# Kernel optimization log

Measured on AMD Instinct MI355X. Metric: run time of the kernel, lower is better.

## Reference

```python
import jax, jax.numpy as jnp
import numpy as np

N_NODES = 50000
N_EDGES = 800000
N_GRAPHS = 512
IN_DIM, HID, OUT_DIM = 128, 96, 10
N_CONV = 4


def setup_inputs() -> dict:
    key = jax.random.key(0)
    ks = jax.random.split(key, 16)
    s = 0.05
    inp = {
        "x": jax.random.normal(ks[0], (N_NODES, IN_DIM), dtype=jnp.float32),
        "edge_index": jax.random.randint(ks[1], (2, N_EDGES), 0, N_NODES, dtype=jnp.int64),
        "batch": jnp.sort(jax.random.randint(ks[2], (N_NODES,), 0, N_GRAPHS, dtype=jnp.int64)),
        # encoder MLP (2 layers: in->hid, hid->hid)
        "enc_W0": jax.random.normal(ks[3], (IN_DIM, HID), dtype=jnp.float32) * s,
        "enc_b0": jnp.zeros((HID,), dtype=jnp.float32),
        "enc_W1": jax.random.normal(ks[4], (HID, HID), dtype=jnp.float32) * s,
        "enc_b1": jnp.zeros((HID,), dtype=jnp.float32),
        # stacked GCNConv weights
        "conv_W": jax.random.normal(ks[5], (N_CONV, HID, HID), dtype=jnp.float32) * s,
        "conv_b": jnp.zeros((N_CONV, HID), dtype=jnp.float32),
        # decoder MLP (2 layers: hid->hid, hid->out)
        "dec_W0": jax.random.normal(ks[6], (HID, HID), dtype=jnp.float32) * s,
        "dec_b0": jnp.zeros((HID,), dtype=jnp.float32),
        "dec_W1": jax.random.normal(ks[7], (HID, OUT_DIM), dtype=jnp.float32) * s,
        "dec_b1": jnp.zeros((OUT_DIM,), dtype=jnp.float32),
    }
    return inp


def reference(x, edge_index, batch, enc_W0, enc_b0, enc_W1, enc_b1,
              conv_W, conv_b, dec_W0, dec_b0, dec_W1, dec_b1):
    n = x.shape[0]
    src, dst = edge_index[0], edge_index[1]  # source_to_target flow

    # encoder MLP (dropout is identity in eval mode)
    h = jax.nn.relu(x @ enc_W0 + enc_b0)
    h = h @ enc_W1 + enc_b1

    # GCN symmetric normalization with self-loops: deg[i] = in_degree + 1
    deg = jax.ops.segment_sum(jnp.ones_like(dst, dtype=h.dtype), dst, num_segments=n) + 1.0
    dinv = jax.lax.rsqrt(deg)                    # [N]
    edge_norm = (dinv[src] * dinv[dst])[:, None]  # [E,1]
    self_norm = (dinv * dinv)[:, None]            # [N,1] self-loop coefficient

    for l in range(conv_W.shape[0]):
        hw = h @ conv_W[l]                              # linear transform [N,HID]
        msg = hw[src] * edge_norm                       # gather + scale [E,HID]
        h = (jax.ops.segment_sum(msg, dst, num_segments=n)
             + hw * self_norm + conv_b[l])              # scatter-add + self-loop + bias
        h = jax.nn.relu(h)

    # global add pool over graphs in the batch
    g = jax.ops.segment_sum(h, batch, num_segments=N_GRAPHS)  # [G,HID]

    # decoder MLP
    g = jax.nn.relu(g @ dec_W0 + dec_b0)
    return g @ dec_W1 + dec_b1
```

## Files before the change

kernel.cpp:

```cpp
#include <hip/hip_runtime.h>

#define HID 96
#define INDIM 128
#define OUTDIM 10

typedef __attribute__((ext_vector_type(8))) short bf16x8;
typedef __attribute__((ext_vector_type(4))) float f32x4;

__device__ __forceinline__ unsigned short f2bf(float f) {
  unsigned int u = __float_as_uint(f);
  unsigned int r = (u + 0x7FFFu + ((u >> 16) & 1u)) >> 16;
  return (unsigned short)r;
}
__device__ __forceinline__ bf16x8 as_bf16x8(uint4 u) {
  union { uint4 a; bf16x8 b; } c; c.a = u; return c.b;
}
__device__ __forceinline__ float bflo(unsigned int u) { return __uint_as_float(u << 16); }
__device__ __forceinline__ float bfhi(unsigned int u) { return __uint_as_float(u & 0xFFFF0000u); }

__global__ __launch_bounds__(256) void k_prep(const float* __restrict__ x,
                                              unsigned int* __restrict__ xb, long long xu,
                                              int* __restrict__ cnt, int n, int XB,
                                              const float* __restrict__ encW0,
                                              const float* __restrict__ encW1,
                                              const float* __restrict__ convW,
                                              uint4* __restrict__ wp) {
  int b = blockIdx.x;
  if (b < XB) {
    long long i = (long long)b * 256 + threadIdx.x;
    if (i < xu) {
      float2 v = ((const float2*)x)[i];
      xb[i] = (unsigned int)f2bf(v.x) | ((unsigned int)f2bf(v.y) << 16);
    }
    if (i < n) cnt[i] = 0;
    return;
  }
  int bid = b - XB;
  int lane = threadIdx.x;
  if (lane >= 64) return;
  const float* Wsrc;
  int frag;
  if (bid < 24) { Wsrc = encW0; frag = bid; }
  else if (bid < 42) { Wsrc = encW1; frag = bid - 24; }
  else { int c = bid - 42; Wsrc = convW + (size_t)(c / 18) * HID * HID; frag = c % 18; }
  int ks = frag / 6, cf = frag % 6;
  int col = cf * 16 + (lane & 15);
  int k0 = ks * 32 + (lane >> 4) * 8;
  unsigned int u[4];
#pragma unroll
  for (int p = 0; p < 4; ++p) {
    float lo = Wsrc[(size_t)(k0 + 2 * p) * 96 + col];
    float hi = Wsrc[(size_t)(k0 + 2 * p + 1) * 96 + col];
    u[p] = (unsigned int)f2bf(lo) | ((unsigned int)f2bf(hi) << 16);
  }
  uint4 r; r.x = u[0]; r.y = u[1]; r.z = u[2]; r.w = u[3];
  wp[(size_t)bid * 64 + lane] = r;
}

__global__ void k_count(const int4* __restrict__ dst4, int E4, int* __restrict__ cnt,
                        int* __restrict__ rank) {
  int i = blockIdx.x * 256 + threadIdx.x;
  if (i >= E4) return;
  int4 d = dst4[i];
  int r0 = atomicAdd(&cnt[d.x], 1);
  int r1 = atomicAdd(&cnt[d.y], 1);
  int r2 = atomicAdd(&cnt[d.z], 1);
  int r3 = atomicAdd(&cnt[d.w], 1);
  ((int4*)rank)[i] = make_int4(r0, r1, r2, r3);
}

__global__ __launch_bounds__(256) void k_scanA(const int* __restrict__ cnt, int n,
                                               int* __restrict__ bsum,
                                               float* __restrict__ dinv) {
  __shared__ int red[256];
  int b = blockIdx.x, t = threadIdx.x;
  int base = b * 512;
  int v = 0;
  int i0 = base + t, i1 = base + 256 + t;
  if (i0 < n) { int c = cnt[i0]; v += c; dinv[i0] = rsqrtf((float)c + 1.0f); }
  if (i1 < n) { int c = cnt[i1]; v += c; dinv[i1] = rsqrtf((float)c + 1.0f); }
  red[t] = v;
  __syncthreads();
  for (int off = 128; off > 0; off >>= 1) {
    if (t < off) red[t] += red[t + off];
    __syncthreads();
  }
  if (t == 0) bsum[b] = red[0];
}

__global__ __launch_bounds__(256) void k_scanB(const int* __restrict__ bsum, int nb,
                                               int* __restrict__ boff,
                                               int* __restrict__ rowp, int n) {
  __shared__ int s[256];
  int t = threadIdx.x;
  int v = (t < nb) ? bsum[t] : 0;
  s[t] = v;
  __syncthreads();
  for (int off = 1; off < 256; off <<= 1) {
    int u = (t >= off) ? s[t - off] : 0;
    __syncthreads();
    s[t] += u;
    __syncthreads();
  }
  if (t < nb) boff[t] = s[t] - v;
  if (t == 255) rowp[n] = s[255];
}

__global__ __launch_bounds__(256) void k_scanC(const int* __restrict__ cnt, int n,
                                               const int* __restrict__ boff,
                                               int* __restrict__ rowp) {
  __shared__ int s[256];
  int b = blockIdx.x, t = threadIdx.x;
  int base = b * 512;
  int i0 = base + 2 * t, i1 = i0 + 1;
  int c0 = (i0 < n) ? cnt[i0] : 0;
  int c1 = (i1 < n) ? cnt[i1] : 0;
  int pair = c0 + c1;
  s[t] = pair;
  __syncthreads();
  for (int off = 1; off < 256; off <<= 1) {
    int u = (t >= off) ? s[t - off] : 0;
    __syncthreads();
    s[t] += u;
    __syncthreads();
  }
  int excl = s[t] - pair + boff[b];
  if (i0 < n) rowp[i0] = excl;
  if (i1 < n) rowp[i1] = excl + c0;
}

__global__ void k_fill(const int4* __restrict__ src4, const int4* __restrict__ dst4,
                       const int4* __restrict__ rank4, int E4,
                       const int* __restrict__ rowp, int* __restrict__ csr) {
  int i = blockIdx.x * 256 + threadIdx.x;
  if (i >= E4) return;
  int4 s = src4[i];
  int4 d = dst4[i];
  int4 r = rank4[i];
  csr[rowp[d.x] + r.x] = s.x;
  csr[rowp[d.y] + r.y] = s.y;
  csr[rowp[d.z] + r.z] = s.z;
  csr[rowp[d.w] + r.w] = s.w;
}

template <int KS, bool RELU, bool BIAS, bool SCALE>
__global__ __launch_bounds__(256) void mfma_gemm(const uint4* __restrict__ Ab,
                                                 const uint4* __restrict__ Bp,
                                                 const float* __restrict__ bias,
                                                 const float* __restrict__ rowscale,
                                                 unsigned int* __restrict__ outB, int M) {
  int t = threadIdx.x, wid = t >> 6, lane = t & 63;
  int rowbase = blockIdx.x * 64 + wid * 16;
  int arow = rowbase + (lane & 15);
  if (arow >= M) arow = M - 1;
  constexpr int RU4 = KS * 4;

  f32x4 acc[6];
#pragma unroll
  for (int cf = 0; cf < 6; ++cf)
#pragma unroll
    for (int j = 0; j < 4; ++j) acc[cf][j] = 0.f;

#pragma unroll
  for (int ks = 0; ks < KS; ++ks) {
    uint4 a = Ab[(size_t)arow * RU4 + ks * 4 + (lane >> 4)];
    bf16x8 af = as_bf16x8(a);
#pragma unroll
    for (int cf = 0; cf < 6; ++cf) {
      uint4 b = Bp[(size_t)(ks * 6 + cf) * 64 + lane];
      acc[cf] = __builtin_amdgcn_mfma_f32_16x16x32_bf16(af, as_bf16x8(b), acc[cf], 0, 0, 0);
    }
  }

  int rows[4]; float rs[4];
#pragma unroll
  for (int i = 0; i < 4; ++i) {
    rows[i] = rowbase + (lane >> 4) * 4 + i;
    int cr = rows[i] < M ? rows[i] : M - 1;
    rs[i] = SCALE ? rowscale[cr] : 1.f;
  }
#pragma unroll
  for (int cf = 0; cf < 6; ++cf) {
    int col = cf * 16 + (lane & 15);
    float bv = BIAS ? bias[col] : 0.f;
#pragma unroll
    for (int i = 0; i < 4; ++i) {
      float v = acc[cf][i] + bv;
      if (RELU) v = fmaxf(v, 0.f);
      v *= rs[i];
      float p = __shfl_xor(v, 1);
      if (!(lane & 1) && rows[i] < M) {
        unsigned int u = (unsigned int)f2bf(v) | ((unsigned int)f2bf(p) << 16);
        outB[(size_t)rows[i] * 48 + cf * 8 + ((lane & 15) >> 1)] = u;
      }
    }
  }
}

__global__ __launch_bounds__(256) void k_agg(const unsigned int* __restrict__ hw_s,
                                             const int* __restrict__ rowp,
                                             const int* __restrict__ csr,
                                             const float* __restrict__ dinv,
                                             const float* __restrict__ bias,
                                             unsigned int* __restrict__ outB, int n) {
  int wave = threadIdx.x >> 6;
  int lane = threadIdx.x & 63;
  int node = blockIdx.x * 4 + wave;
  if (node >= n) return;
  int beg = rowp[node], end = rowp[node + 1];
  float acc0 = 0.f, acc1 = 0.f;
  bool act = lane < 48;
  int li = act ? lane : 0;
  int e = beg;
  for (; e + 8 <= end; e += 8) {
    unsigned int u0 = hw_s[(size_t)csr[e + 0] * 48 + li];
    unsigned int u1 = hw_s[(size_t)csr[e + 1] * 48 + li];
    unsigned int u2 = hw_s[(size_t)csr[e + 2] * 48 + li];
    unsigned int u3 = hw_s[(size_t)csr[e + 3] * 48 + li];
    unsigned int u4 = hw_s[(size_t)csr[e + 4] * 48 + li];
    unsigned int u5 = hw_s[(size_t)csr[e + 5] * 48 + li];
    unsigned int u6 = hw_s[(size_t)csr[e + 6] * 48 + li];
    unsigned int u7 = hw_s[(size_t)csr[e + 7] * 48 + li];
    acc0 += bflo(u0) + bflo(u1) + bflo(u2) + bflo(u3) +
            bflo(u4) + bflo(u5) + bflo(u6) + bflo(u7);
    acc1 += bfhi(u0) + bfhi(u1) + bfhi(u2) + bfhi(u3) +
            bfhi(u4) + bfhi(u5) + bfhi(u6) + bfhi(u7);
  }
  for (; e + 4 <= end; e += 4) {
    unsigned int u0 = hw_s[(size_t)csr[e + 0] * 48 + li];
    unsigned int u1 = hw_s[(size_t)csr[e + 1] * 48 + li];
    unsigned int u2 = hw_s[(size_t)csr[e + 2] * 48 + li];
    unsigned int u3 = hw_s[(size_t)csr[e + 3] * 48 + li];
    acc0 += bflo(u0) + bflo(u1) + bflo(u2) + bflo(u3);
    acc1 += bfhi(u0) + bfhi(u1) + bfhi(u2) + bfhi(u3);
  }
  for (; e < end; ++e) {
    unsigned int u = hw_s[(size_t)csr[e] * 48 + li];
    acc0 += bflo(u);
    acc1 += bfhi(u);
  }
  if (act) {
    float di = dinv[node];
    unsigned int us = hw_s[(size_t)node * 48 + li];
    float2 bv = ((const float2*)bias)[li];
    float r0 = fmaxf(di * (acc0 + bflo(us)) + bv.x, 0.f);
    float r1 = fmaxf(di * (acc1 + bfhi(us)) + bv.y, 0.f);
    outB[(size_t)node * 48 + li] = (unsigned int)f2bf(r0) | ((unsigned int)f2bf(r1) << 16);
  }
}

__global__ __launch_bounds__(256) void k_head(const unsigned int* __restrict__ hb,
                                              const int* __restrict__ batch, int n,
                                              const float* __restrict__ W0,
                                              const float* __restrict__ b0,
                                              const float* __restrict__ W1,
                                              const float* __restrict__ b1,
                                              float* __restrict__ out) {
  __shared__ float w0L[HID * HID];
  __shared__ float red[4][HID];
  __shared__ float g1L[HID];
  __shared__ float g2L[HID];
  int gr = blockIdx.x;
  int t = threadIdx.x, wv = t >> 6, lane = t & 63;

  for (int i = t; i < HID * HID / 4; i += 256) ((float4*)w0L)[i] = ((const float4*)W0)[i];

  int lo = 0, hi = n;
  while (lo < hi) { int m = (lo + hi) >> 1; if (batch[m] < gr) lo = m + 1; else hi = m; }
  int start = lo;
  hi = n;
  while (lo < hi) { int m = (lo + hi) >> 1; if (batch[m] < gr + 1) lo = m + 1; else hi = m; }
  int end = lo;

  if (lane < 48) {
    float s0 = 0.f, s1 = 0.f;
    for (int i = start + wv; i < end; i += 4) {
      unsigned int u = hb[(size_t)i * 48 + lane];
      s0 += bflo(u);
      s1 += bfhi(u);
    }
    red[wv][2 * lane] = s0;
    red[wv][2 * lane + 1] = s1;
  }
  __syncthreads();
  if (t < HID) g1L[t] = red[0][t] + red[1][t] + red[2][t] + red[3][t];
  __syncthreads();
  if (t < HID) {
    float a = b0[t];
    for (int k = 0; k < HID; ++k) a += g1L[k] * w0L[k * HID + t];
    g2L[t] = fmaxf(a, 0.f);
  }
  __syncthreads();
  if (t < OUTDIM) {
    float a = b1[t];
    for (int k = 0; k < HID; ++k) a += g2L[k] * W1[k * OUTDIM + t];
    out[(size_t)gr * OUTDIM + t] = a;
  }
}

extern "C" void kernel_launch(void* const* d_in, const int* in_sizes, int n_in,
                              void* d_out, int out_size, void* d_ws, size_t ws_size,
                              hipStream_t stream) {
  const float* x     = (const float*)d_in[0];
  const int*   ei    = (const int*)d_in[1];
  const int*   batch = (const int*)d_in[2];
  const float* encW0 = (const float*)d_in[3];
  const float* encb0 = (const float*)d_in[4];
  const float* encW1 = (const float*)d_in[5];
  const float* encb1 = (const float*)d_in[6];
  const float* convW = (const float*)d_in[7];
  const float* convb = (const float*)d_in[8];
  const float* decW0 = (const float*)d_in[9];
  const float* decb0 = (const float*)d_in[10];
  const float* decW1 = (const float*)d_in[11];
  const float* decb1 = (const float*)d_in[12];
  float* out = (float*)d_out;

  int n  = in_sizes[0] / INDIM;
  int E  = in_sizes[1] / 2;
  int G  = out_size / OUTDIM;
  int NC = in_sizes[7] / (HID * HID);

  const int* srcI = ei;
  const int* dstI = ei + E;

  char* w = (char*)d_ws;
  auto alloc = [&](size_t bytes) {
    char* p = w;
    w += (bytes + 255) & ~(size_t)255;
    return p;
  };
  unsigned int* xb  = (unsigned int*)alloc((size_t)n * (INDIM / 2) * 4);
  unsigned int* hbA = (unsigned int*)alloc((size_t)n * 48 * 4);
  unsigned int* hbB = (unsigned int*)alloc((size_t)n * 48 * 4);
  unsigned int* hwb = (unsigned int*)alloc((size_t)n * 48 * 4);
  uint4* wp   = (uint4*)alloc((size_t)(42 + NC * 18) * 64 * 16);
  int*   cnt   = (int*)alloc((size_t)n * 4);
  int*   rankb = (int*)alloc((size_t)E * 4);
  int*   rowp  = (int*)alloc((size_t)(n + 1) * 4);
  int*   csr   = (int*)alloc((size_t)E * 4);
  float* dinv  = (float*)alloc((size_t)n * 4);
  int*   bsum  = (int*)alloc(256 * 4);
  int*   boff  = (int*)alloc(256 * 4);

  long long xu = (long long)n * (INDIM / 2);
  int XB = (int)((xu + 255) / 256);
  int WB = 42 + NC * 18;
  k_prep<<<XB + WB, 256, 0, stream>>>(x, xb, xu, cnt, n, XB, encW0, encW1, convW, wp);

  int E4 = E / 4;
  int eb4 = (E4 + 255) / 256;
  int nb = (n + 511) / 512;
  k_count<<<eb4, 256, 0, stream>>>((const int4*)dstI, E4, cnt, rankb);
  k_scanA<<<nb, 256, 0, stream>>>(cnt, n, bsum, dinv);
  k_scanB<<<1, 256, 0, stream>>>(bsum, nb, boff, rowp, n);
  k_scanC<<<nb, 256, 0, stream>>>(cnt, n, boff, rowp);
  k_fill<<<eb4, 256, 0, stream>>>((const int4*)srcI, (const int4*)dstI,
                                  (const int4*)rankb, E4, rowp, csr);

  int gb = (n + 63) / 64;
  mfma_gemm<4, true, true, false><<<gb, 256, 0, stream>>>(
      (const uint4*)xb, wp, encb0, nullptr, hbA, n);
  mfma_gemm<3, false, true, false><<<gb, 256, 0, stream>>>(
      (const uint4*)hbA, wp + (size_t)24 * 64, encb1, nullptr, hbB, n);
  for (int l = 0; l < NC; ++l) {
    mfma_gemm<3, false, false, true><<<gb, 256, 0, stream>>>(
        (const uint4*)hbB, wp + (size_t)(42 + l * 18) * 64, nullptr, dinv, hwb, n);
    k_agg<<<(n + 3) / 4, 256, 0, stream>>>(hwb, rowp, csr, dinv,
                                           convb + (size_t)l * HID, hbB, n);
  }
  k_head<<<G, 256, 0, stream>>>(hbB, batch, n, decW0, decb0, decW1, decb1, out);
}
```

Baseline: 276.7 us.

## Co-schedule CSR build stages with encoder and first conv GEMMs in merged launches

Graph preprocessing kernels (count, scanA, scanC) are merged with independent dense GEMMs (encoder layers and the first conv transform) into combined grids, using block-index dispatch. This removes three launches and lets the latency-bound atomic and scan work overlap with MFMA work. The aggregation inner loop is also widened from 8 to 16 gathered neighbors per iteration for more memory-level parallelism. The cost is higher register pressure in the aggregation kernel, and mixed-role blocks sharing one launch configuration.

```diff
diff --git a/kernel.cpp b/kernel.cpp
--- a/kernel.cpp
+++ b/kernel.cpp
@@ -57,9 +57,9 @@
   wp[(size_t)bid * 64 + lane] = r;
 }
 
-__global__ void k_count(const int4* __restrict__ dst4, int E4, int* __restrict__ cnt,
-                        int* __restrict__ rank) {
-  int i = blockIdx.x * 256 + threadIdx.x;
+__device__ __forceinline__ void count_body(int blk, const int4* __restrict__ dst4, int E4,
+                                           int* __restrict__ cnt, int* __restrict__ rank) {
+  int i = blk * 256 + threadIdx.x;
   if (i >= E4) return;
   int4 d = dst4[i];
   int r0 = atomicAdd(&cnt[d.x], 1);
@@ -69,12 +69,11 @@
   ((int4*)rank)[i] = make_int4(r0, r1, r2, r3);
 }
 
-__global__ __launch_bounds__(256) void k_scanA(const int* __restrict__ cnt, int n,
-                                               int* __restrict__ bsum,
-                                               float* __restrict__ dinv) {
+__device__ __forceinline__ void scanA_body(int blk, const int* __restrict__ cnt, int n,
+                                           int* __restrict__ bsum, float* __restrict__ dinv) {
   __shared__ int red[256];
-  int b = blockIdx.x, t = threadIdx.x;
-  int base = b * 512;
+  int t = threadIdx.x;
+  int base = blk * 512;
   int v = 0;
   int i0 = base + t, i1 = base + 256 + t;
   if (i0 < n) { int c = cnt[i0]; v += c; dinv[i0] = rsqrtf((float)c + 1.0f); }
@@ -85,7 +84,121 @@
     if (t < off) red[t] += red[t + off];
     __syncthreads();
   }
-  if (t == 0) bsum[b] = red[0];
+  if (t == 0) bsum[blk] = red[0];
+}
+
+__device__ __forceinline__ void scanC_body(int blk, const int* __restrict__ cnt, int n,
+                                           const int* __restrict__ boff,
+                                           int* __restrict__ rowp) {
+  __shared__ int s[256];
+  int t = threadIdx.x;
+  int base = blk * 512;
+  int i0 = base + 2 * t, i1 = i0 + 1;
+  int c0 = (i0 < n) ? cnt[i0] : 0;
+  int c1 = (i1 < n) ? cnt[i1] : 0;
+  int pair = c0 + c1;
+  s[t] = pair;
+  __syncthreads();
+  for (int off = 1; off < 256; off <<= 1) {
+    int u = (t >= off) ? s[t - off] : 0;
+    __syncthreads();
+    s[t] += u;
+    __syncthreads();
+  }
+  int excl = s[t] - pair + boff[blk];
+  if (i0 < n) rowp[i0] = excl;
+  if (i1 < n) rowp[i1] = excl + c0;
+}
+
+template <int KS, bool RELU, bool BIAS, bool SCALE>
+__device__ __forceinline__ void gemm_body(int blk, const uint4* __restrict__ Ab,
+                                          const uint4* __restrict__ Bp,
+                                          const float* __restrict__ bias,
+                                          const float* __restrict__ rowscale,
+                                          unsigned int* __restrict__ outB, int M) {
+  int t = threadIdx.x, wid = t >> 6, lane = t & 63;
+  int rowbase = blk * 64 + wid * 16;
+  int arow = rowbase + (lane & 15);
+  if (arow >= M) arow = M - 1;
+  constexpr int RU4 = KS * 4;
+
+  f32x4 acc[6];
+#pragma unroll
+  for (int cf = 0; cf < 6; ++cf)
+#pragma unroll
+    for (int j = 0; j < 4; ++j) acc[cf][j] = 0.f;
+
+#pragma unroll
+  for (int ks = 0; ks < KS; ++ks) {
+    uint4 a = Ab[(size_t)arow * RU4 + ks * 4 + (lane >> 4)];
+    bf16x8 af = as_bf16x8(a);
+#pragma unroll
+    for (int cf = 0; cf < 6; ++cf) {
+      uint4 b = Bp[(size_t)(ks * 6 + cf) * 64 + lane];
+      acc[cf] = __builtin_amdgcn_mfma_f32_16x16x32_bf16(af, as_bf16x8(b), acc[cf], 0, 0, 0);
+    }
+  }
+
+  int rows[4]; float rs[4];
+#pragma unroll
+  for (int i = 0; i < 4; ++i) {
+    rows[i] = rowbase + (lane >> 4) * 4 + i;
+    int cr = rows[i] < M ? rows[i] : M - 1;
+    rs[i] = SCALE ? rowscale[cr] : 1.f;
+  }
+#pragma unroll
+  for (int cf = 0; cf < 6; ++cf) {
+    int col = cf * 16 + (lane & 15);
+    float bv = BIAS ? bias[col] : 0.f;
+#pragma unroll
+    for (int i = 0; i < 4; ++i) {
+      float v = acc[cf][i] + bv;
+      if (RELU) v = fmaxf(v, 0.f);
+      v *= rs[i];
+      float p = __shfl_xor(v, 1);
+      if (!(lane & 1) && rows[i] < M) {
+        unsigned int u = (unsigned int)f2bf(v) | ((unsigned int)f2bf(p) << 16);
+        outB[(size_t)rows[i] * 48 + cf * 8 + ((lane & 15) >> 1)] = u;
+      }
+    }
+  }
+}
+
+__global__ __launch_bounds__(256) void k_count_enc1(
+    const int4* __restrict__ dst4, int E4, int* __restrict__ cnt, int* __restrict__ rank,
+    int CB, const uint4* __restrict__ Ab, const uint4* __restrict__ Bp,
+    const float* __restrict__ bias, unsigned int* __restrict__ outB, int M) {
+  int b = blockIdx.x;
+  if (b < CB) count_body(b, dst4, E4, cnt, rank);
+  else gemm_body<4, true, true, false>(b - CB, Ab, Bp, bias, nullptr, outB, M);
+}
+
+__global__ __launch_bounds__(256) void k_scanA_enc2(
+    const int* __restrict__ cnt, int n, int* __restrict__ bsum, float* __restrict__ dinv,
+    int SB, const uint4* __restrict__ Ab, const uint4* __restrict__ Bp,
+    const float* __restrict__ bias, unsigned int* __restrict__ outB, int M) {
+  int b = blockIdx.x;
+  if (b < SB) scanA_body(b, cnt, n, bsum, dinv);
+  else gemm_body<3, false, true, false>(b - SB, Ab, Bp, bias, nullptr, outB, M);
+}
+
+__global__ __launch_bounds__(256) void k_scanC_conv(
+    const int* __restrict__ cnt, int n, const int* __restrict__ boff,
+    int* __restrict__ rowp, int SB, const uint4* __restrict__ Ab,
+    const uint4* __restrict__ Bp, const float* __restrict__ rowscale,
+    unsigned int* __restrict__ outB, int M) {
+  int b = blockIdx.x;
+  if (b < SB) scanC_body(b, cnt, n, boff, rowp);
+  else gemm_body<3, false, false, true>(b - SB, Ab, Bp, nullptr, rowscale, outB, M);
+}
+
+template <int KS, bool RELU, bool BIAS, bool SCALE>
+__global__ __launch_bounds__(256) void mfma_gemm(const uint4* __restrict__ Ab,
+                                                 const uint4* __restrict__ Bp,
+                                                 const float* __restrict__ bias,
+                                                 const float* __restrict__ rowscale,
+                                                 unsigned int* __restrict__ outB, int M) {
+  gemm_body<KS, RELU, BIAS, SCALE>(blockIdx.x, Ab, Bp, bias, rowscale, outB, M);
 }
 
 __global__ __launch_bounds__(256) void k_scanB(const int* __restrict__ bsum, int nb,
@@ -104,29 +217,6 @@
   }
   if (t < nb) boff[t] = s[t] - v;
   if (t == 255) rowp[n] = s[255];
-}
-
-__global__ __launch_bounds__(256) void k_scanC(const int* __restrict__ cnt, int n,
-                                               const int* __restrict__ boff,
-                                               int* __restrict__ rowp) {
-  __shared__ int s[256];
-  int b = blockIdx.x, t = threadIdx.x;
-  int base = b * 512;
-  int i0 = base + 2 * t, i1 = i0 + 1;
-  int c0 = (i0 < n) ? cnt[i0] : 0;
-  int c1 = (i1 < n) ? cnt[i1] : 0;
-  int pair = c0 + c1;
-  s[t] = pair;
-  __syncthreads();
-  for (int off = 1; off < 256; off <<= 1) {
-    int u = (t >= off) ? s[t - off] : 0;
-    __syncthreads();
-    s[t] += u;
-    __syncthreads();
-  }
-  int excl = s[t] - pair + boff[b];
-  if (i0 < n) rowp[i0] = excl;
-  if (i1 < n) rowp[i1] = excl + c0;
 }
 
 __global__ void k_fill(const int4* __restrict__ src4, const int4* __restrict__ dst4,
@@ -141,60 +231,6 @@
   csr[rowp[d.y] + r.y] = s.y;
   csr[rowp[d.z] + r.z] = s.z;
   csr[rowp[d.w] + r.w] = s.w;
-}
-
-template <int KS, bool RELU, bool BIAS, bool SCALE>
-__global__ __launch_bounds__(256) void mfma_gemm(const uint4* __restrict__ Ab,
-                                                 const uint4* __restrict__ Bp,
-                                                 const float* __restrict__ bias,
-                                                 const float* __restrict__ rowscale,
-                                                 unsigned int* __restrict__ outB, int M) {
-  int t = threadIdx.x, wid = t >> 6, lane = t & 63;
-  int rowbase = blockIdx.x * 64 + wid * 16;
-  int arow = rowbase + (lane & 15);
-  if (arow >= M) arow = M - 1;
-  constexpr int RU4 = KS * 4;
-
-  f32x4 acc[6];
-#pragma unroll
-  for (int cf = 0; cf < 6; ++cf)
-#pragma unroll
-    for (int j = 0; j < 4; ++j) acc[cf][j] = 0.f;
-
-#pragma unroll
-  for (int ks = 0; ks < KS; ++ks) {
-    uint4 a = Ab[(size_t)arow * RU4 + ks * 4 + (lane >> 4)];
-    bf16x8 af = as_bf16x8(a);
-#pragma unroll
-    for (int cf = 0; cf < 6; ++cf) {
-      uint4 b = Bp[(size_t)(ks * 6 + cf) * 64 + lane];
-      acc[cf] = __builtin_amdgcn_mfma_f32_16x16x32_bf16(af, as_bf16x8(b), acc[cf], 0, 0, 0);
-    }
-  }
-
-  int rows[4]; float rs[4];
-#pragma unroll
-  for (int i = 0; i < 4; ++i) {
-    rows[i] = rowbase + (lane >> 4) * 4 + i;
-    int cr = rows[i] < M ? rows[i] : M - 1;
-    rs[i] = SCALE ? rowscale[cr] : 1.f;
-  }
-#pragma unroll
-  for (int cf = 0; cf < 6; ++cf) {
-    int col = cf * 16 + (lane & 15);
-    float bv = BIAS ? bias[col] : 0.f;
-#pragma unroll
-    for (int i = 0; i < 4; ++i) {
-      float v = acc[cf][i] + bv;
-      if (RELU) v = fmaxf(v, 0.f);
-      v *= rs[i];
-      float p = __shfl_xor(v, 1);
-      if (!(lane & 1) && rows[i] < M) {
-        unsigned int u = (unsigned int)f2bf(v) | ((unsigned int)f2bf(p) << 16);
-        outB[(size_t)rows[i] * 48 + cf * 8 + ((lane & 15) >> 1)] = u;
-      }
-    }
-  }
 }
 
 __global__ __launch_bounds__(256) void k_agg(const unsigned int* __restrict__ hw_s,
@@ -212,19 +248,14 @@
   bool act = lane < 48;
   int li = act ? lane : 0;
   int e = beg;
-  for (; e + 8 <= end; e += 8) {
-    unsigned int u0 = hw_s[(size_t)csr[e + 0] * 48 + li];
-    unsigned int u1 = hw_s[(size_t)csr[e + 1] * 48 + li];
-    unsigned int u2 = hw_s[(size_t)csr[e + 2] * 48 + li];
-    unsigned int u3 = hw_s[(size_t)csr[e + 3] * 48 + li];
-    unsigned int u4 = hw_s[(size_t)csr[e + 4] * 48 + li];
-    unsigned int u5 = hw_s[(size_t)csr[e + 5] * 48 + li];
-    unsigned int u6 = hw_s[(size_t)csr[e + 6] * 48 + li];
-    unsigned int u7 = hw_s[(size_t)csr[e + 7] * 48 + li];
-    acc0 += bflo(u0) + bflo(u1) + bflo(u2) + bflo(u3) +
-            bflo(u4) + bflo(u5) + bflo(u6) + bflo(u7);
-    acc1 += bfhi(u0) + bfhi(u1) + bfhi(u2) + bfhi(u3) +
-            bfhi(u4) + bfhi(u5) + bfhi(u6) + bfhi(u7);
+  for (; e + 16 <= end; e += 16) {
+    unsigned int uu[16];
+#pragma unroll
+    for (int j = 0; j < 16; ++j) uu[j] = hw_s[(size_t)csr[e + j] * 48 + li];
+    float a0 = 0.f, a1 = 0.f;
+#pragma unroll
+    for (int j = 0; j < 16; ++j) { a0 += bflo(uu[j]); a1 += bfhi(uu[j]); }
+    acc0 += a0; acc1 += a1;
   }
   for (; e + 4 <= end; e += 4) {
     unsigned int u0 = hw_s[(size_t)csr[e + 0] * 48 + li];
@@ -351,19 +382,22 @@
   int E4 = E / 4;
   int eb4 = (E4 + 255) / 256;
   int nb = (n + 511) / 512;
-  k_count<<<eb4, 256, 0, stream>>>((const int4*)dstI, E4, cnt, rankb);
-  k_scanA<<<nb, 256, 0, stream>>>(cnt, n, bsum, dinv);
+  int gb = (n + 63) / 64;
+
+  k_count_enc1<<<eb4 + gb, 256, 0, stream>>>((const int4*)dstI, E4, cnt, rankb, eb4,
+                                             (const uint4*)xb, wp, encb0, hbA, n);
+  k_scanA_enc2<<<nb + gb, 256, 0, stream>>>(cnt, n, bsum, dinv, nb,
+                                            (const uint4*)hbA, wp + (size_t)24 * 64,
+                                            encb1, hbB, n);
   k_scanB<<<1, 256, 0, stream>>>(bsum, nb, boff, rowp, n);
-  k_scanC<<<nb, 256, 0, stream>>>(cnt, n, boff, rowp);
+  k_scanC_conv<<<nb + gb, 256, 0, stream>>>(cnt, n, boff, rowp, nb,
+                                            (const uint4*)hbB, wp + (size_t)42 * 64,
+                                            dinv, hwb, n);
   k_fill<<<eb4, 256, 0, stream>>>((const int4*)srcI, (const int4*)dstI,
                                   (const int4*)rankb, E4, rowp, csr);
-
-  int gb = (n + 63) / 64;
-  mfma_gemm<4, true, true, false><<<gb, 256, 0, stream>>>(
-      (const uint4*)xb, wp, encb0, nullptr, hbA, n);
-  mfma_gemm<3, false, true, false><<<gb, 256, 0, stream>>>(
-      (const uint4*)hbA, wp + (size_t)24 * 64, encb1, nullptr, hbB, n);
-  for (int l = 0; l < NC; ++l) {
+  k_agg<<<(n + 3) / 4, 256, 0, stream>>>(hwb, rowp, csr, dinv, convb, hbB, n);
+
+  for (int l = 1; l < NC; ++l) {
     mfma_gemm<3, false, false, true><<<gb, 256, 0, stream>>>(
         (const uint4*)hbB, wp + (size_t)(42 + l * 18) * 64, nullptr, dinv, hwb, n);
     k_agg<<<(n + 3) / 4, 256, 0, stream>>>(hwb, rowp, csr, dinv,
```

Result: faster. 270.2 us (-2.3%).
